# Performance work log

Measured on AMD Instinct MI355X. Metric: run time of the kernel, lower is better.

Reference implementation:

```python
import jax, jax.numpy as jnp
import numpy as np

KH, KW = 3, 3
STRIDE = (1, 1)
PAD = (1, 1)
DIL = (1, 1)
DG = 1  # num_deformable_groups


def _out_size(h, pad, dil, k, stride):
    return (h + 2 * pad - (dil * (k - 1) + 1)) // stride + 1


def setup_inputs() -> dict:
    key = jax.random.key(0)
    k1, k2, k3 = jax.random.split(key, 3)
    B, Cin, H, W = 8, 128, 64, 64
    Cout = 128
    Ho = _out_size(H, PAD[0], DIL[0], KH, STRIDE[0])
    Wo = _out_size(W, PAD[1], DIL[1], KW, STRIDE[1])
    x = jax.random.normal(k1, (B, Cin, H, W), jnp.float32)
    offset = jax.random.normal(k2, (B, 2 * DG * KH * KW, Ho, Wo), jnp.float32)
    n = Cin * KH * KW
    stdv = 1.0 / np.sqrt(n)
    weight = jax.random.uniform(k3, (Cout, Cin, KH, KW), jnp.float32, -stdv, stdv)
    return {"x": x, "offset": offset, "weight": weight}


def deform_conv2d(x, offset, weight):
    B, Cin, H, W = x.shape
    Cout, _, kh, kw = weight.shape
    K = kh * kw
    Ho = _out_size(H, PAD[0], DIL[0], kh, STRIDE[0])
    Wo = _out_size(W, PAD[1], DIL[1], kw, STRIDE[1])
    G = DG
    Cg = Cin // G

    # base sampling grid per kernel tap: [kh,kw,Ho,Wo]
    by = (jnp.arange(kh) * DIL[0])[:, None, None, None] + (jnp.arange(Ho) * STRIDE[0] - PAD[0])[None, None, :, None]
    bx = (jnp.arange(kw) * DIL[1])[None, :, None, None] + (jnp.arange(Wo) * STRIDE[1] - PAD[1])[None, None, None, :]
    by = jnp.broadcast_to(by, (kh, kw, Ho, Wo)).reshape(K, Ho, Wo).astype(x.dtype)
    bx = jnp.broadcast_to(bx, (kh, kw, Ho, Wo)).reshape(K, Ho, Wo).astype(x.dtype)

    # offset layout: channel = g*2*K + 2*k + {0: dy, 1: dx}
    off = offset.reshape(B, G, K, 2, Ho, Wo)
    py = by[None, None] + off[:, :, :, 0]  # [B,G,K,Ho,Wo]
    px = bx[None, None] + off[:, :, :, 1]

    y0 = jnp.floor(py).astype(jnp.int32)
    x0 = jnp.floor(px).astype(jnp.int32)
    wy = (py - y0).reshape(B, G, 1, -1)  # fractional parts, [B,G,1,K*Ho*Wo]
    wx = (px - x0).reshape(B, G, 1, -1)

    xg = x.reshape(B, G, Cg, H * W)
    N = K * Ho * Wo

    def gather(yi, xi):
        valid = ((yi >= 0) & (yi < H) & (xi >= 0) & (xi < W)).reshape(B, G, 1, N)
        idx = (jnp.clip(yi, 0, H - 1) * W + jnp.clip(xi, 0, W - 1)).reshape(B, G, 1, N)
        v = jnp.take_along_axis(xg, jnp.broadcast_to(idx, (B, G, Cg, N)), axis=3)
        return v * valid.astype(x.dtype)

    v00 = gather(y0, x0)
    v01 = gather(y0, x0 + 1)
    v10 = gather(y0 + 1, x0)
    v11 = gather(y0 + 1, x0 + 1)

    cols = (v00 * (1 - wy) * (1 - wx) + v01 * (1 - wy) * wx
            + v10 * wy * (1 - wx) + v11 * wy * wx)
    cols = cols.reshape(B, G, Cg, K, Ho, Wo)  # deformable im2col columns

    wr = weight.reshape(Cout, G, Cg, K)
    return jnp.einsum('ogck,bgcknm->bonm', wr, cols)


def reference(x, offset, weight):
    return deform_conv2d(x, offset, weight)
```

## Files before the change

### kernel.cpp

```cpp
#include <hip/hip_runtime.h>
#include <hip/hip_fp16.h>

typedef __attribute__((ext_vector_type(4))) float f32x4;
typedef __attribute__((ext_vector_type(8))) _Float16 f16x8;
typedef __attribute__((ext_vector_type(4))) unsigned int u32x4;

__device__ __forceinline__ unsigned short f2h(float f) {
  __half h = __float2half_rn(f);
  unsigned short u;
  __builtin_memcpy(&u, &h, 2);
  return u;
}
__device__ __forceinline__ __half2 h2_of(unsigned int u) {
  __half2 h;
  __builtin_memcpy(&h, &u, 4);
  return h;
}
__device__ __forceinline__ unsigned int u_of(__half2 h) {
  unsigned int u;
  __builtin_memcpy(&u, &h, 4);
  return u;
}

__global__ __launch_bounds__(256) void prep_kernel(const float* __restrict__ x,
                                                   const float* __restrict__ w,
                                                   unsigned short* __restrict__ xt,
                                                   unsigned short* __restrict__ wf) {
  if (blockIdx.x < 2048) {
    int t = blockIdx.x * 256 + threadIdx.x;
    int p  = t & 4095;
    int cg = (t >> 12) & 15;
    int b  = t >> 16;
    const float* xp = x + (((size_t)(b * 128 + cg * 8)) << 12) + p;
    unsigned int r[8];
#pragma unroll
    for (int j = 0; j < 8; ++j) r[j] = f2h(xp[(size_t)j << 12]);
    u32x4 pk;
    pk.x = r[0] | (r[1] << 16);
    pk.y = r[2] | (r[3] << 16);
    pk.z = r[4] | (r[5] << 16);
    pk.w = r[6] | (r[7] << 16);
    *reinterpret_cast<u32x4*>(xt + ((((size_t)b << 12) + p) << 7) + cg * 8) = pk;
  } else {
    int tid = (blockIdx.x - 2048) * 256 + threadIdx.x;
    int l  = tid & 63;
    int mt = (tid >> 6) & 7;
    int ch = tid >> 9;
    int cc = ch / 9, tap = ch - cc * 9;
    int co = mt * 16 + (l & 15);
    int cb = cc * 32 + (l >> 4) * 8;
    unsigned int r[8];
#pragma unroll
    for (int j = 0; j < 8; ++j)
      r[j] = f2h(w[(co * 128 + cb + j) * 9 + tap]);
    u32x4 pk;
    pk.x = r[0] | (r[1] << 16);
    pk.y = r[2] | (r[3] << 16);
    pk.z = r[4] | (r[5] << 16);
    pk.w = r[6] | (r[7] << 16);
    *reinterpret_cast<u32x4*>(wf + (size_t)tid * 8) = pk;
  }
}

__global__ __launch_bounds__(512, 1) void deform_kernel(const unsigned short* __restrict__ xt,
                                                        const float* __restrict__ off,
                                                        const unsigned short* __restrict__ wf,
                                                        float* __restrict__ out) {
  __shared__ __align__(16) unsigned char sWin[8 * 17408];
  __shared__ int   sPos[1152];
  __shared__ uint2 sWt[1152];

  const int tid = threadIdx.x;
  const int bid = blockIdx.x;
  const int b   = bid & 7;
  const int ho0 = (bid >> 3) * 2;
  const int r0  = min(max(ho0 - 3, 0), 56);

  {
    const unsigned short* xrow = xt + ((size_t)b << 19) + ((size_t)r0 << 13);
#pragma unroll
    for (int it = 0; it < 16; ++it) {
      int idx = it * 512 + tid;
      int c = idx & 15;
      int p = (idx >> 4) & 63;
      int r = idx >> 10;
      u32x4 v;
      __builtin_memcpy(&v, xrow + (((size_t)(r * 64 + p)) << 7) + c * 8, 16);
      *reinterpret_cast<u32x4*>(&sWin[r * 17408 + p * 272 + c * 16]) = v;
    }
  }

  for (int r = tid; r < 1152; r += 512) {
    int row = (r >= 576) ? 1 : 0;
    int rr  = r - row * 576;
    int tap = rr >> 6, wo = rr & 63;
    int ho = ho0 + row;
    float dy = off[((b * 18 + 2 * tap)     * 64 + ho) * 64 + wo];
    float dx = off[((b * 18 + 2 * tap + 1) * 64 + ho) * 64 + wo];
    float py = (float)(ho + (tap / 3) - 1) + dy;
    float px = (float)(wo + (tap % 3) - 1) + dx;
    float fy = floorf(py), fx = floorf(px);
    int y0 = (int)fy, x0 = (int)fx;
    float wy = py - fy, wx = px - fx;
    float wt = (y0 >= 0 && y0 < 64) ? (1.f - wy) : 0.f;
    float wb = (y0 + 1 >= 0 && y0 + 1 < 64) ? wy : 0.f;
    int y0c = min(max(y0, 0), 63), y1c = min(max(y0 + 1, 0), 63);
    int bx; float wl, wr;
    if (x0 >= 0 && x0 <= 62)      { bx = x0; wl = 1.f - wx; wr = wx;       }
    else if (x0 == -1)            { bx = 0;  wl = wx;       wr = 0.f;      }
    else if (x0 == 63)            { bx = 62; wl = 0.f;      wr = 1.f - wx; }
    else                          { bx = 0;  wl = 0.f;      wr = 0.f;      }
    sPos[r] = (y0c * 64 + bx) | ((y1c != y0c) ? (1 << 15) : 0);
    __half2 tp = __floats2half2_rn(wt * wl, wt * wr);
    __half2 bp = __floats2half2_rn(wb * wl, wb * wr);
    uint2 ww;
    ww.x = u_of(tp);
    ww.y = u_of(bp);
    sWt[r] = ww;
  }
  __syncthreads();

  const int l   = tid & 63;
  const int w   = tid >> 6;
  const int ks  = w & 3;
  const int row = w >> 2;
  const int ln  = l & 15;
  const int kg  = l >> 4;
  const int koff = ks * 64 + kg * 16;
  const int ho  = ho0 + row;

  const unsigned short* xtb = xt + ((size_t)b << 19) + ks * 32 + kg * 8;
  const unsigned short* wfb = wf + (size_t)l * 8;

  f32x4 acc[4][8] = {};

  for (int tap = 0; tap < 9; ++tap) {
    const int ch = ks * 9 + tap;

    f16x8 A[8];
    const unsigned short* wp = wfb + (size_t)(ch * 8) * 512;
#pragma unroll
    for (int mt = 0; mt < 8; ++mt)
      A[mt] = *reinterpret_cast<const f16x8*>(wp + (size_t)mt * 512);

    u32x4 T0[4], T1[4], B0[4], B1[4];
    uint2 wws[4];
#pragma unroll
    for (int pg = 0; pg < 4; ++pg) {
      const int e = row * 576 + tap * 64 + pg * 16 + ln;
      const int pp = sPos[e];
      wws[pg] = sWt[e];

      const int aX = pp & 4095;
      const int aY = aX + ((pp >> 9) & 64);
      const int tx  = aX & 63;
      const int twr = (aX >> 6) - r0;
      const int bwr = (aY >> 6) - r0;
      const bool tin = (unsigned)twr < 8u;
      const bool bin = (unsigned)bwr < 8u;

      const int laT = (tin ? twr : 0) * 17408 + tx * 272 + koff;
      __builtin_memcpy(&T0[pg], &sWin[laT],       16);
      __builtin_memcpy(&T1[pg], &sWin[laT + 272], 16);
      const int laB = (bin ? bwr : 0) * 17408 + tx * 272 + koff;
      __builtin_memcpy(&B0[pg], &sWin[laB],       16);
      __builtin_memcpy(&B1[pg], &sWin[laB + 272], 16);

      if (!tin) {
        const unsigned short* p0 = xtb + ((size_t)aX << 7);
        __builtin_memcpy(&T0[pg], p0,       16);
        __builtin_memcpy(&T1[pg], p0 + 128, 16);
      }
      if (!bin) {
        const unsigned short* p1 = xtb + ((size_t)aY << 7);
        __builtin_memcpy(&B0[pg], p1,       16);
        __builtin_memcpy(&B1[pg], p1 + 128, 16);
      }
    }

#pragma unroll
    for (int pg = 0; pg < 4; ++pg) {
      const uint2 ww = wws[pg];
      const __half2 wtl = __half2half2(__low2half(h2_of(ww.x)));
      const __half2 wtr = __half2half2(__high2half(h2_of(ww.x)));
      const __half2 wbl = __half2half2(__low2half(h2_of(ww.y)));
      const __half2 wbr = __half2half2(__high2half(h2_of(ww.y)));
      u32x4 pk;
#pragma unroll
      for (int d = 0; d < 4; ++d) {
        __half2 s = __hmul2(wtl, h2_of(T0[pg][d]));
        s = __hfma2(wtr, h2_of(T1[pg][d]), s);
        s = __hfma2(wbl, h2_of(B0[pg][d]), s);
        s = __hfma2(wbr, h2_of(B1[pg][d]), s);
        pk[d] = u_of(s);
      }
      f16x8 bfrag;
      __builtin_memcpy(&bfrag, &pk, 16);

#pragma unroll
      for (int mt = 0; mt < 8; ++mt)
        acc[pg][mt] = __builtin_amdgcn_mfma_f32_16x16x32_f16(A[mt], bfrag,
                                                             acc[pg][mt], 0, 0, 0);
    }
  }

  float* sF = reinterpret_cast<float*>(sWin);
#define WR_LDS(BASE)                                                           \
  { _Pragma("unroll") for (int pg = 0; pg < 4; ++pg)                           \
    _Pragma("unroll") for (int mt = 0; mt < 8; ++mt)                           \
      *reinterpret_cast<f32x4*>(&sF[(BASE) + row * 8448 + (pg * 16 + ln) * 132 + mt * 16 + kg * 4]) = acc[pg][mt]; }
#define RD_LDS(BASE)                                                           \
  { _Pragma("unroll") for (int pg = 0; pg < 4; ++pg)                           \
    _Pragma("unroll") for (int mt = 0; mt < 8; ++mt) {                         \
      f32x4 v = *reinterpret_cast<const f32x4*>(&sF[(BASE) + row * 8448 + (pg * 16 + ln) * 132 + mt * 16 + kg * 4]); \
      acc[pg][mt] += v; } }

  __syncthreads();
  if (ks == 1) WR_LDS(17408)
  if (ks == 3) WR_LDS(0)
  __syncthreads();
  if (ks == 0) RD_LDS(17408)
  if (ks == 2) RD_LDS(0)
  __syncthreads();
  if (ks == 2) WR_LDS(17408)
  __syncthreads();
  if (ks == 0) RD_LDS(17408)
#undef WR_LDS
#undef RD_LDS

  {
    const int b2 = row * 8704;
    if (ks == 0) {
#pragma unroll
      for (int pg = 0; pg < 4; ++pg)
#pragma unroll
        for (int mt = 0; mt < 8; ++mt)
#pragma unroll
          for (int rg = 0; rg < 4; ++rg)
            sF[b2 + (mt * 16 + kg * 4 + rg) * 68 + pg * 16 + ln] = acc[pg][mt][rg];
    }
    __syncthreads();
    if (ks == 0) {
      const int q4  = l & 15;
      const int ch2 = l >> 4;
      float* ob = out + (((size_t)b * 128) * 64 + ho) * 64 + q4 * 4;
#pragma unroll
      for (int i = 0; i < 32; ++i) {
        int co = ch2 * 32 + i;
        f32x4 v = *reinterpret_cast<const f32x4*>(&sF[b2 + co * 68 + q4 * 4]);
        *reinterpret_cast<f32x4*>(ob + (size_t)co * 4096) = v;
      }
    }
  }
}

extern "C" void kernel_launch(void* const* d_in, const int* in_sizes, int n_in,
                              void* d_out, int out_size, void* d_ws, size_t ws_size,
                              hipStream_t stream) {
  (void)in_sizes; (void)n_in; (void)out_size; (void)ws_size;
  const float* x   = (const float*)d_in[0];
  const float* off = (const float*)d_in[1];
  const float* w   = (const float*)d_in[2];
  float* out = (float*)d_out;
  unsigned short* xt = (unsigned short*)d_ws;
  unsigned short* wf = (unsigned short*)d_ws + (8388608 / 2);

  prep_kernel<<<2120, 256, 0, stream>>>(x, w, xt, wf);
  deform_kernel<<<256, 512, 0, stream>>>(xt, off, wf, out);
}
```

Measured before the change: 100.1 us.

## Fuse x fp16 transpose into deform kernel window load, drop xt workspace

The separate pass that converted x to a channel-last fp16 copy in workspace is removed. The deform kernel now reads fp32 x directly when filling its shared-memory row window, converting and packing to fp16 on the fly. Out-of-window samples fall back to strided fp32 global reads. Per-sample shared addresses are also precomputed into a packed int2 with an out-of-window flag. This saves a full write and reread of an intermediate tensor, but the window fill becomes strided scalar loads with redundant reads across blocks, and the fallback path gets more expensive.

```diff
diff --git a/kernel.cpp b/kernel.cpp
--- a/kernel.cpp
+++ b/kernel.cpp
@@ -22,52 +22,33 @@
   return u;
 }
 
-__global__ __launch_bounds__(256) void prep_kernel(const float* __restrict__ x,
-                                                   const float* __restrict__ w,
-                                                   unsigned short* __restrict__ xt,
+__global__ __launch_bounds__(256) void prep_kernel(const float* __restrict__ w,
                                                    unsigned short* __restrict__ wf) {
-  if (blockIdx.x < 2048) {
-    int t = blockIdx.x * 256 + threadIdx.x;
-    int p  = t & 4095;
-    int cg = (t >> 12) & 15;
-    int b  = t >> 16;
-    const float* xp = x + (((size_t)(b * 128 + cg * 8)) << 12) + p;
-    unsigned int r[8];
-#pragma unroll
-    for (int j = 0; j < 8; ++j) r[j] = f2h(xp[(size_t)j << 12]);
-    u32x4 pk;
-    pk.x = r[0] | (r[1] << 16);
-    pk.y = r[2] | (r[3] << 16);
-    pk.z = r[4] | (r[5] << 16);
-    pk.w = r[6] | (r[7] << 16);
-    *reinterpret_cast<u32x4*>(xt + ((((size_t)b << 12) + p) << 7) + cg * 8) = pk;
-  } else {
-    int tid = (blockIdx.x - 2048) * 256 + threadIdx.x;
-    int l  = tid & 63;
-    int mt = (tid >> 6) & 7;
-    int ch = tid >> 9;
-    int cc = ch / 9, tap = ch - cc * 9;
-    int co = mt * 16 + (l & 15);
-    int cb = cc * 32 + (l >> 4) * 8;
-    unsigned int r[8];
-#pragma unroll
-    for (int j = 0; j < 8; ++j)
-      r[j] = f2h(w[(co * 128 + cb + j) * 9 + tap]);
-    u32x4 pk;
-    pk.x = r[0] | (r[1] << 16);
-    pk.y = r[2] | (r[3] << 16);
-    pk.z = r[4] | (r[5] << 16);
-    pk.w = r[6] | (r[7] << 16);
-    *reinterpret_cast<u32x4*>(wf + (size_t)tid * 8) = pk;
-  }
-}
-
-__global__ __launch_bounds__(512, 1) void deform_kernel(const unsigned short* __restrict__ xt,
+  int tid = blockIdx.x * 256 + threadIdx.x;
+  int l  = tid & 63;
+  int mt = (tid >> 6) & 7;
+  int ch = tid >> 9;
+  int cc = ch / 9, tap = ch - cc * 9;
+  int co = mt * 16 + (l & 15);
+  int cb = cc * 32 + (l >> 4) * 8;
+  unsigned int r[8];
+#pragma unroll
+  for (int j = 0; j < 8; ++j)
+    r[j] = f2h(w[(co * 128 + cb + j) * 9 + tap]);
+  u32x4 pk;
+  pk.x = r[0] | (r[1] << 16);
+  pk.y = r[2] | (r[3] << 16);
+  pk.z = r[4] | (r[5] << 16);
+  pk.w = r[6] | (r[7] << 16);
+  *reinterpret_cast<u32x4*>(wf + (size_t)tid * 8) = pk;
+}
+
+__global__ __launch_bounds__(512, 1) void deform_kernel(const float* __restrict__ x,
                                                         const float* __restrict__ off,
                                                         const unsigned short* __restrict__ wf,
                                                         float* __restrict__ out) {
   __shared__ __align__(16) unsigned char sWin[8 * 17408];
-  __shared__ int   sPos[1152];
+  __shared__ int2  sPA[1152];
   __shared__ uint2 sWt[1152];
 
   const int tid = threadIdx.x;
@@ -77,16 +58,23 @@
   const int r0  = min(max(ho0 - 3, 0), 56);
 
   {
-    const unsigned short* xrow = xt + ((size_t)b << 19) + ((size_t)r0 << 13);
+    const float* xb = x + ((size_t)b << 19) + ((size_t)r0 << 6);
 #pragma unroll
     for (int it = 0; it < 16; ++it) {
       int idx = it * 512 + tid;
-      int c = idx & 15;
-      int p = (idx >> 4) & 63;
-      int r = idx >> 10;
-      u32x4 v;
-      __builtin_memcpy(&v, xrow + (((size_t)(r * 64 + p)) << 7) + c * 8, 16);
-      *reinterpret_cast<u32x4*>(&sWin[r * 17408 + p * 272 + c * 16]) = v;
+      int p  = idx & 63;
+      int r  = (idx >> 6) & 7;
+      int cg = idx >> 9;
+      const float* xp = xb + (((size_t)cg) << 15) + (r << 6) + p;
+      unsigned int q[8];
+#pragma unroll
+      for (int j = 0; j < 8; ++j) q[j] = f2h(xp[(size_t)j << 12]);
+      u32x4 pk;
+      pk.x = q[0] | (q[1] << 16);
+      pk.y = q[2] | (q[3] << 16);
+      pk.z = q[4] | (q[5] << 16);
+      pk.w = q[6] | (q[7] << 16);
+      *reinterpret_cast<u32x4*>(&sWin[r * 17408 + p * 272 + cg * 16]) = pk;
     }
   }
 
@@ -110,7 +98,16 @@
     else if (x0 == -1)            { bx = 0;  wl = wx;       wr = 0.f;      }
     else if (x0 == 63)            { bx = 62; wl = 0.f;      wr = 1.f - wx; }
     else                          { bx = 0;  wl = 0.f;      wr = 0.f;      }
-    sPos[r] = (y0c * 64 + bx) | ((y1c != y0c) ? (1 << 15) : 0);
+    int aX = y0c * 64 + bx, aY = y1c * 64 + bx;
+    int twr = y0c - r0, bwr = y1c - r0;
+    int tin = ((unsigned)twr < 8u) ? 1 : 0;
+    int bin = ((unsigned)bwr < 8u) ? 1 : 0;
+    int laT0 = (tin ? twr : 0) * 17408 + bx * 272;
+    int laB0 = (bin ? bwr : 0) * 17408 + bx * 272;
+    int2 pw;
+    pw.x = laT0 | (aX << 18) | (tin ? 0 : (int)0x80000000);
+    pw.y = laB0 | (aY << 18) | (bin ? 0 : (int)0x80000000);
+    sPA[r] = pw;
     __half2 tp = __floats2half2_rn(wt * wl, wt * wr);
     __half2 bp = __floats2half2_rn(wb * wl, wb * wr);
     uint2 ww;
@@ -129,7 +126,7 @@
   const int koff = ks * 64 + kg * 16;
   const int ho  = ho0 + row;
 
-  const unsigned short* xtb = xt + ((size_t)b << 19) + ks * 32 + kg * 8;
+  const float* xfb = x + ((size_t)b << 19) + (((size_t)(ks * 32 + kg * 8)) << 12);
   const unsigned short* wfb = wf + (size_t)l * 8;
 
   f32x4 acc[4][8] = {};
@@ -148,33 +145,47 @@
 #pragma unroll
     for (int pg = 0; pg < 4; ++pg) {
       const int e = row * 576 + tap * 64 + pg * 16 + ln;
-      const int pp = sPos[e];
+      const int2 pa = sPA[e];
       wws[pg] = sWt[e];
 
-      const int aX = pp & 4095;
-      const int aY = aX + ((pp >> 9) & 64);
-      const int tx  = aX & 63;
-      const int twr = (aX >> 6) - r0;
-      const int bwr = (aY >> 6) - r0;
-      const bool tin = (unsigned)twr < 8u;
-      const bool bin = (unsigned)bwr < 8u;
-
-      const int laT = (tin ? twr : 0) * 17408 + tx * 272 + koff;
+      const int laT = (pa.x & 0x3FFFF) + koff;
       __builtin_memcpy(&T0[pg], &sWin[laT],       16);
       __builtin_memcpy(&T1[pg], &sWin[laT + 272], 16);
-      const int laB = (bin ? bwr : 0) * 17408 + tx * 272 + koff;
+      const int laB = (pa.y & 0x3FFFF) + koff;
       __builtin_memcpy(&B0[pg], &sWin[laB],       16);
       __builtin_memcpy(&B1[pg], &sWin[laB + 272], 16);
 
-      if (!tin) {
-        const unsigned short* p0 = xtb + ((size_t)aX << 7);
-        __builtin_memcpy(&T0[pg], p0,       16);
-        __builtin_memcpy(&T1[pg], p0 + 128, 16);
-      }
-      if (!bin) {
-        const unsigned short* p1 = xtb + ((size_t)aY << 7);
-        __builtin_memcpy(&B0[pg], p1,       16);
-        __builtin_memcpy(&B1[pg], p1 + 128, 16);
+      if (pa.x < 0) {
+        const int aX = (pa.x >> 18) & 4095;
+        const float* p0 = xfb + aX;
+        u32x4 q0, q1;
+#pragma unroll
+        for (int d = 0; d < 4; ++d) {
+          unsigned int a0 = f2h(p0[(size_t)(2 * d)     << 12]);
+          unsigned int a1 = f2h(p0[(size_t)(2 * d + 1) << 12]);
+          q0[d] = a0 | (a1 << 16);
+          unsigned int c0 = f2h(p0[((size_t)(2 * d)     << 12) + 1]);
+          unsigned int c1 = f2h(p0[((size_t)(2 * d + 1) << 12) + 1]);
+          q1[d] = c0 | (c1 << 16);
+        }
+        T0[pg] = q0;
+        T1[pg] = q1;
+      }
+      if (pa.y < 0) {
+        const int aY = (pa.y >> 18) & 4095;
+        const float* p1 = xfb + aY;
+        u32x4 q0, q1;
+#pragma unroll
+        for (int d = 0; d < 4; ++d) {
+          unsigned int a0 = f2h(p1[(size_t)(2 * d)     << 12]);
+          unsigned int a1 = f2h(p1[(size_t)(2 * d + 1) << 12]);
+          q0[d] = a0 | (a1 << 16);
+          unsigned int c0 = f2h(p1[((size_t)(2 * d)     << 12) + 1]);
+          unsigned int c1 = f2h(p1[((size_t)(2 * d + 1) << 12) + 1]);
+          q1[d] = c0 | (c1 << 16);
+        }
+        B0[pg] = q0;
+        B1[pg] = q1;
       }
     }
 
@@ -262,9 +273,8 @@
   const float* off = (const float*)d_in[1];
   const float* w   = (const float*)d_in[2];
   float* out = (float*)d_out;
-  unsigned short* xt = (unsigned short*)d_ws;
-  unsigned short* wf = (unsigned short*)d_ws + (8388608 / 2);
-
-  prep_kernel<<<2120, 256, 0, stream>>>(x, w, xt, wf);
-  deform_kernel<<<256, 512, 0, stream>>>(xt, off, wf, out);
-}
+  unsigned short* wf = (unsigned short*)d_ws;
+
+  prep_kernel<<<72, 256, 0, stream>>>(w, wf);
+  deform_kernel<<<256, 512, 0, stream>>>(x, off, wf, out);
+}
```

After: 97.72 us. 2.4% less time.
